# Kernel tuning notes

Measured on AMD Instinct MI355X. Metric: run time of the kernel, lower is better.

Reference implementation:

```python
import jax, jax.numpy as jnp
import numpy as np

ND = 64       # dijetFeatures (channels)
NPAIR = 6     # six dijet slots


def _interleave(x, d):
    # x: [n, nd, 12] -> [n, nd, 6, 2]; d: [n, nd, 6] -> [n, nd, 6, 1]
    n, nd, _ = x.shape
    xr = x.reshape(n, nd, NPAIR, 2)
    z = jnp.concatenate([xr, d[..., None]], axis=-1)  # [n, nd, 6, 3]
    return z


def _conv_s3(z, W, b):
    # z: [n, in, 6, 3] grouped windows; W: [out, in, 3]; stride-3 k-3 conv == per-window contraction
    return jnp.einsum('bisk,oik->bos', z, W) + b[None, :, None]  # [n, out, 6]


def setup_inputs() -> dict:
    key = jax.random.key(0)
    ks = jax.random.split(key, 8)
    n = 65536
    inp = {
        'x': jax.random.normal(ks[0], (n, ND, 12), dtype=jnp.float32),
        'd': jax.random.normal(ks[1], (n, ND, NPAIR), dtype=jnp.float32),
        'W1': jax.random.normal(ks[2], (ND, ND, 3), dtype=jnp.float32) * 0.05,
        'b1': jax.random.normal(ks[3], (ND,), dtype=jnp.float32) * 0.05,
        'W2': jax.random.normal(ks[4], (ND, ND, 3), dtype=jnp.float32) * 0.05,
        'b2': jax.random.normal(ks[5], (ND,), dtype=jnp.float32) * 0.05,
        'W3': jax.random.normal(ks[6], (ND, ND, 3), dtype=jnp.float32) * 0.05,
        'b3': jax.random.normal(ks[7], (ND,), dtype=jnp.float32) * 0.05,
    }
    return inp


def reference(x, d, W1, b1, W2, b2, W3, b3):
    d1 = d
    d = jax.nn.relu(_conv_s3(_interleave(x, d), W1, b1))
    d = jax.nn.relu(_conv_s3(_interleave(x, d), W2, b2))
    d = _conv_s3(_interleave(x, d), W3, b3)
    return jax.nn.relu(d + d1)
```

## Files before the change

### kernel.cpp

```cpp
#include <hip/hip_runtime.h>

#define ND 64
#define NPAIR 6

typedef short bf16x8 __attribute__((ext_vector_type(8)));
typedef float floatx4 __attribute__((ext_vector_type(4)));

static constexpr int SPB  = 16;
static constexpr int ROWS = SPB * NPAIR;
static constexpr int ASTR = 200;

__device__ __forceinline__ unsigned short f2bf(float f) {
    unsigned u = __builtin_bit_cast(unsigned, f);
    u += 0x7FFFu + ((u >> 16) & 1u);
    return (unsigned short)(u >> 16);
}
__device__ __forceinline__ unsigned f2bf2(float lo, float hi) {
    return (unsigned)f2bf(lo) | ((unsigned)f2bf(hi) << 16);
}

__global__ void repack_w(const float* __restrict__ W1, const float* __restrict__ W2,
                         const float* __restrict__ W3, unsigned short* __restrict__ P) {
    int idx = blockIdx.x * 256 + threadIdx.x;
    if (idx >= 3 * 64 * 192) return;
    int j = idx % 192;
    int n = (idx / 192) % 64;
    int L = idx / (192 * 64);
    const float* W = (L == 0) ? W1 : (L == 1) ? W2 : W3;
    float v = (j < 128) ? W[n * 192 + (j >> 1) * 3 + (j & 1)]
                        : W[n * 192 + (j - 128) * 3 + 2];
    P[idx] = f2bf(v);
}

__global__ __launch_bounds__(256, 4) void dijet_main(
    const float* __restrict__ x, const float* __restrict__ d,
    const float* __restrict__ b1, const float* __restrict__ b2,
    const float* __restrict__ b3, const unsigned short* __restrict__ Wp,
    float* __restrict__ out)
{
    __shared__ __align__(16) unsigned short A[ROWS * ASTR];
    float* Ct = (float*)A;

    const int t  = threadIdx.x;
    const int b0 = blockIdx.x * SPB;

    {
        const float4* x4 = (const float4*)(x + (size_t)b0 * (ND * 12));
        unsigned* A32 = (unsigned*)A;
        #pragma unroll
        for (int half = 0; half < 2; ++half) {
            float4 v[6];
            #pragma unroll
            for (int m = 0; m < 6; ++m) v[m] = x4[(half * 6 + m) * 256 + t];
            #pragma unroll
            for (int m = 0; m < 6; ++m) {
                int idx = (half * 6 + m) * 256 + t;
                int b   = idx / 192;
                int rem = idx - b * 192;
                int i   = rem / 3;
                int c0  = (rem - i * 3) * 4;
                int row0 = b * 6 + (c0 >> 1);
                A32[row0 * (ASTR / 2) + i]       = f2bf2(v[m].x, v[m].y);
                A32[(row0 + 1) * (ASTR / 2) + i] = f2bf2(v[m].z, v[m].w);
            }
        }
    }
    {
        const float2* d2 = (const float2*)(d + (size_t)b0 * (ND * NPAIR));
        #pragma unroll
        for (int half = 0; half < 2; ++half) {
            float2 v[6];
            #pragma unroll
            for (int m = 0; m < 6; ++m) v[m] = d2[(half * 6 + m) * 256 + t];
            #pragma unroll
            for (int m = 0; m < 6; ++m) {
                int idx = (half * 6 + m) * 256 + t;
                int e   = idx * 2;
                int b   = e / 384;
                int rem = e - b * 384;
                int i   = rem / 6;
                int s   = rem - i * 6;
                int row = b * 6 + s;
                A[row * ASTR + 128 + i]       = f2bf(v[m].x);
                A[(row + 1) * ASTR + 128 + i] = f2bf(v[m].y);
            }
        }
    }
    __syncthreads();

    const int wave = t >> 6;
    const int lane = t & 63;
    const int mhalf = wave & 1;
    const int nhalf = wave >> 1;
    const int l15  = lane & 15;
    const int quad = lane >> 4;

    const int mbase = mhalf * 48;
    const int nbase = nhalf * 32;

    #pragma unroll
    for (int L = 0; L < 3; ++L) {
        const float* bL = (L == 0) ? b1 : (L == 1) ? b2 : b3;
        const unsigned short* WL = Wp + L * (64 * 192);

        bf16x8 Bf[2][6];
        #pragma unroll
        for (int nt = 0; nt < 2; ++nt)
            #pragma unroll
            for (int kk = 0; kk < 6; ++kk)
                Bf[nt][kk] = *(const bf16x8*)(WL + (nbase + nt * 16 + l15) * 192 + kk * 32 + quad * 8);
        float bias0 = bL[nbase + l15];
        float bias1 = bL[nbase + 16 + l15];

        floatx4 acc[3][2] = {};
        #pragma unroll
        for (int kk = 0; kk < 6; ++kk) {
            #pragma unroll
            for (int mt = 0; mt < 3; ++mt) {
                bf16x8 Af = *(const bf16x8*)(A + (mbase + mt * 16 + l15) * ASTR + kk * 32 + quad * 8);
                acc[mt][0] = __builtin_amdgcn_mfma_f32_16x16x32_bf16(Af, Bf[0][kk], acc[mt][0], 0, 0, 0);
                acc[mt][1] = __builtin_amdgcn_mfma_f32_16x16x32_bf16(Af, Bf[1][kk], acc[mt][1], 0, 0, 0);
            }
        }

        if (L < 2) {
            __syncthreads();
            #pragma unroll
            for (int mt = 0; mt < 3; ++mt) {
                #pragma unroll
                for (int nt = 0; nt < 2; ++nt) {
                    float bias = nt ? bias1 : bias0;
                    int o = nbase + nt * 16 + l15;
                    #pragma unroll
                    for (int r = 0; r < 4; ++r) {
                        int row = mbase + mt * 16 + quad * 4 + r;
                        float v = acc[mt][nt][r] + bias;
                        v = v > 0.f ? v : 0.f;
                        A[row * ASTR + 128 + o] = f2bf(v);
                    }
                }
            }
            __syncthreads();
        } else {
            __syncthreads();
            #pragma unroll
            for (int mt = 0; mt < 3; ++mt) {
                #pragma unroll
                for (int nt = 0; nt < 2; ++nt) {
                    float bias = nt ? bias1 : bias0;
                    int o = nbase + nt * 16 + l15;
                    #pragma unroll
                    for (int r = 0; r < 4; ++r) {
                        int row = mbase + mt * 16 + quad * 4 + r;
                        int bl  = row / 6;
                        int s   = row - bl * 6;
                        Ct[bl * (ND * NPAIR) + o * NPAIR + s] = acc[mt][nt][r] + bias;
                    }
                }
            }
            __syncthreads();
            const float4* dres4 = (const float4*)(d + (size_t)b0 * (ND * NPAIR));
            float4*       out4  = (float4*)(out + (size_t)b0 * (ND * NPAIR));
            const float4* Ct4   = (const float4*)Ct;
            #pragma unroll
            for (int m = 0; m < 6; ++m) {
                int idx = m * 256 + t;
                float4 c = Ct4[idx];
                float4 dv = dres4[idx];
                float4 r;
                r.x = c.x + dv.x; r.x = r.x > 0.f ? r.x : 0.f;
                r.y = c.y + dv.y; r.y = r.y > 0.f ? r.y : 0.f;
                r.z = c.z + dv.z; r.z = r.z > 0.f ? r.z : 0.f;
                r.w = c.w + dv.w; r.w = r.w > 0.f ? r.w : 0.f;
                out4[idx] = r;
            }
        }
    }
}

extern "C" void kernel_launch(void* const* d_in, const int* in_sizes, int n_in,
                              void* d_out, int out_size, void* d_ws, size_t ws_size,
                              hipStream_t stream)
{
    const float* x  = (const float*)d_in[0];
    const float* dd = (const float*)d_in[1];
    const float* W1 = (const float*)d_in[2];
    const float* b1 = (const float*)d_in[3];
    const float* W2 = (const float*)d_in[4];
    const float* b2 = (const float*)d_in[5];
    const float* W3 = (const float*)d_in[6];
    const float* b3 = (const float*)d_in[7];
    float* out = (float*)d_out;
    unsigned short* Wp = (unsigned short*)d_ws;

    int n = in_sizes[0] / (ND * 12);

    repack_w<<<144, 256, 0, stream>>>(W1, W2, W3, Wp);
    dijet_main<<<n / SPB, 256, 0, stream>>>(x, dd, b1, b2, b3, Wp, out);
}
```

Measured before the change: 421.7 us.

## Halve samples per block, keep residual d in registers, raise occupancy

Cuts samples per block from 16 to 8, halving the LDS tile. Each wave now covers all 48 rows for a 16-column output slice instead of a 48x32 quadrant, and launch bounds rise to 7 blocks per SIMD. The residual d values are loaded once into registers and reused for the final add, so the second global read of d is gone. The intent is more resident blocks to hide memory latency and less global traffic. The cost is more blocks, each reloading the packed weights, and smaller per-wave MFMA tiles.

```diff
diff --git a/kernel.cpp b/kernel.cpp
--- a/kernel.cpp
+++ b/kernel.cpp
@@ -6,7 +6,7 @@
 typedef short bf16x8 __attribute__((ext_vector_type(8)));
 typedef float floatx4 __attribute__((ext_vector_type(4)));
 
-static constexpr int SPB  = 16;
+static constexpr int SPB  = 8;
 static constexpr int ROWS = SPB * NPAIR;
 static constexpr int ASTR = 200;
 
@@ -32,7 +32,7 @@
     P[idx] = f2bf(v);
 }
 
-__global__ __launch_bounds__(256, 4) void dijet_main(
+__global__ __launch_bounds__(256, 7) void dijet_main(
     const float* __restrict__ x, const float* __restrict__ d,
     const float* __restrict__ b1, const float* __restrict__ b2,
     const float* __restrict__ b3, const unsigned short* __restrict__ Wp,
@@ -44,100 +44,84 @@
     const int t  = threadIdx.x;
     const int b0 = blockIdx.x * SPB;
 
+    float2 dres[6];
+    {
+        const float2* d2 = (const float2*)(d + (size_t)b0 * (ND * NPAIR));
+        #pragma unroll
+        for (int m = 0; m < 6; ++m) dres[m] = d2[m * 256 + t];
+    }
     {
         const float4* x4 = (const float4*)(x + (size_t)b0 * (ND * 12));
+        float4 v[6];
+        #pragma unroll
+        for (int m = 0; m < 6; ++m) v[m] = x4[m * 256 + t];
         unsigned* A32 = (unsigned*)A;
         #pragma unroll
-        for (int half = 0; half < 2; ++half) {
-            float4 v[6];
-            #pragma unroll
-            for (int m = 0; m < 6; ++m) v[m] = x4[(half * 6 + m) * 256 + t];
-            #pragma unroll
-            for (int m = 0; m < 6; ++m) {
-                int idx = (half * 6 + m) * 256 + t;
-                int b   = idx / 192;
-                int rem = idx - b * 192;
-                int i   = rem / 3;
-                int c0  = (rem - i * 3) * 4;
-                int row0 = b * 6 + (c0 >> 1);
-                A32[row0 * (ASTR / 2) + i]       = f2bf2(v[m].x, v[m].y);
-                A32[(row0 + 1) * (ASTR / 2) + i] = f2bf2(v[m].z, v[m].w);
-            }
+        for (int m = 0; m < 6; ++m) {
+            int idx = m * 256 + t;
+            int b   = idx / 192;
+            int rem = idx - b * 192;
+            int i   = rem / 3;
+            int c0  = (rem - i * 3) * 4;
+            int row0 = b * 6 + (c0 >> 1);
+            A32[row0 * (ASTR / 2) + i]       = f2bf2(v[m].x, v[m].y);
+            A32[(row0 + 1) * (ASTR / 2) + i] = f2bf2(v[m].z, v[m].w);
         }
     }
     {
-        const float2* d2 = (const float2*)(d + (size_t)b0 * (ND * NPAIR));
         #pragma unroll
-        for (int half = 0; half < 2; ++half) {
-            float2 v[6];
-            #pragma unroll
-            for (int m = 0; m < 6; ++m) v[m] = d2[(half * 6 + m) * 256 + t];
-            #pragma unroll
-            for (int m = 0; m < 6; ++m) {
-                int idx = (half * 6 + m) * 256 + t;
-                int e   = idx * 2;
-                int b   = e / 384;
-                int rem = e - b * 384;
-                int i   = rem / 6;
-                int s   = rem - i * 6;
-                int row = b * 6 + s;
-                A[row * ASTR + 128 + i]       = f2bf(v[m].x);
-                A[(row + 1) * ASTR + 128 + i] = f2bf(v[m].y);
-            }
+        for (int m = 0; m < 6; ++m) {
+            int idx = m * 256 + t;
+            int e   = idx * 2;
+            int b   = e / 384;
+            int rem = e - b * 384;
+            int i   = rem / 6;
+            int s   = rem - i * 6;
+            int row = b * 6 + s;
+            A[row * ASTR + 128 + i]       = f2bf(dres[m].x);
+            A[(row + 1) * ASTR + 128 + i] = f2bf(dres[m].y);
         }
     }
     __syncthreads();
 
     const int wave = t >> 6;
     const int lane = t & 63;
-    const int mhalf = wave & 1;
-    const int nhalf = wave >> 1;
     const int l15  = lane & 15;
     const int quad = lane >> 4;
-
-    const int mbase = mhalf * 48;
-    const int nbase = nhalf * 32;
+    const int nbase = wave * 16;
 
     #pragma unroll
     for (int L = 0; L < 3; ++L) {
         const float* bL = (L == 0) ? b1 : (L == 1) ? b2 : b3;
         const unsigned short* WL = Wp + L * (64 * 192);
 
-        bf16x8 Bf[2][6];
+        bf16x8 Bf[6];
         #pragma unroll
-        for (int nt = 0; nt < 2; ++nt)
-            #pragma unroll
-            for (int kk = 0; kk < 6; ++kk)
-                Bf[nt][kk] = *(const bf16x8*)(WL + (nbase + nt * 16 + l15) * 192 + kk * 32 + quad * 8);
-        float bias0 = bL[nbase + l15];
-        float bias1 = bL[nbase + 16 + l15];
+        for (int kk = 0; kk < 6; ++kk)
+            Bf[kk] = *(const bf16x8*)(WL + (nbase + l15) * 192 + kk * 32 + quad * 8);
+        float bias = bL[nbase + l15];
 
-        floatx4 acc[3][2] = {};
+        floatx4 acc[3] = {};
         #pragma unroll
         for (int kk = 0; kk < 6; ++kk) {
             #pragma unroll
             for (int mt = 0; mt < 3; ++mt) {
-                bf16x8 Af = *(const bf16x8*)(A + (mbase + mt * 16 + l15) * ASTR + kk * 32 + quad * 8);
-                acc[mt][0] = __builtin_amdgcn_mfma_f32_16x16x32_bf16(Af, Bf[0][kk], acc[mt][0], 0, 0, 0);
-                acc[mt][1] = __builtin_amdgcn_mfma_f32_16x16x32_bf16(Af, Bf[1][kk], acc[mt][1], 0, 0, 0);
+                bf16x8 Af = *(const bf16x8*)(A + (mt * 16 + l15) * ASTR + kk * 32 + quad * 8);
+                acc[mt] = __builtin_amdgcn_mfma_f32_16x16x32_bf16(Af, Bf[kk], acc[mt], 0, 0, 0);
             }
         }
 
+        const int o = nbase + l15;
         if (L < 2) {
             __syncthreads();
             #pragma unroll
             for (int mt = 0; mt < 3; ++mt) {
                 #pragma unroll
-                for (int nt = 0; nt < 2; ++nt) {
-                    float bias = nt ? bias1 : bias0;
-                    int o = nbase + nt * 16 + l15;
-                    #pragma unroll
-                    for (int r = 0; r < 4; ++r) {
-                        int row = mbase + mt * 16 + quad * 4 + r;
-                        float v = acc[mt][nt][r] + bias;
-                        v = v > 0.f ? v : 0.f;
-                        A[row * ASTR + 128 + o] = f2bf(v);
-                    }
+                for (int r = 0; r < 4; ++r) {
+                    int row = mt * 16 + quad * 4 + r;
+                    float v = acc[mt][r] + bias;
+                    v = v > 0.f ? v : 0.f;
+                    A[row * ASTR + 128 + o] = f2bf(v);
                 }
             }
             __syncthreads();
@@ -146,33 +130,24 @@
             #pragma unroll
             for (int mt = 0; mt < 3; ++mt) {
                 #pragma unroll
-                for (int nt = 0; nt < 2; ++nt) {
-                    float bias = nt ? bias1 : bias0;
-                    int o = nbase + nt * 16 + l15;
-                    #pragma unroll
-                    for (int r = 0; r < 4; ++r) {
-                        int row = mbase + mt * 16 + quad * 4 + r;
-                        int bl  = row / 6;
-                        int s   = row - bl * 6;
-                        Ct[bl * (ND * NPAIR) + o * NPAIR + s] = acc[mt][nt][r] + bias;
-                    }
+                for (int r = 0; r < 4; ++r) {
+                    int row = mt * 16 + quad * 4 + r;
+                    int bl  = row / 6;
+                    int s   = row - bl * 6;
+                    Ct[bl * (ND * NPAIR) + o * NPAIR + s] = acc[mt][r] + bias;
                 }
             }
             __syncthreads();
-            const float4* dres4 = (const float4*)(d + (size_t)b0 * (ND * NPAIR));
-            float4*       out4  = (float4*)(out + (size_t)b0 * (ND * NPAIR));
-            const float4* Ct4   = (const float4*)Ct;
+            float2* out2 = (float2*)(out + (size_t)b0 * (ND * NPAIR));
+            const float2* Ct2 = (const float2*)Ct;
             #pragma unroll
             for (int m = 0; m < 6; ++m) {
                 int idx = m * 256 + t;
-                float4 c = Ct4[idx];
-                float4 dv = dres4[idx];
-                float4 r;
-                r.x = c.x + dv.x; r.x = r.x > 0.f ? r.x : 0.f;
-                r.y = c.y + dv.y; r.y = r.y > 0.f ? r.y : 0.f;
-                r.z = c.z + dv.z; r.z = r.z > 0.f ? r.z : 0.f;
-                r.w = c.w + dv.w; r.w = r.w > 0.f ? r.w : 0.f;
-                out4[idx] = r;
+                float2 c = Ct2[idx];
+                float2 r;
+                r.x = c.x + dres[m].x; r.x = r.x > 0.f ? r.x : 0.f;
+                r.y = c.y + dres[m].y; r.y = r.y > 0.f ? r.y : 0.f;
+                out2[idx] = r;
             }
         }
     }
```

New measurement: 390.7 us. 7.3% less time.
